# Kernel tuning notes

Hardware: AMD Instinct MI355X
Metric: run time of the kernel (lower is better)

The kernel has to match this reference:

```python
import jax, jax.numpy as jnp
import numpy as np

SCALE = 0.08838834764831845  # 1/sqrt(head_dim=128)
B, H, HKV, D = 32, 32, 8, 128
NUM_BLOCKS, BLOCK_SIZE, MAX_NUM_BLOCKS = 4096, 16, 256


def setup_inputs() -> dict:
    key = jax.random.key(0)
    ks = jax.random.split(key, 8)
    q = jax.random.normal(ks[0], (B, H, D), dtype=jnp.float32)
    k = jax.random.normal(ks[1], (B, HKV, D), dtype=jnp.float32)
    v = jax.random.normal(ks[2], (B, HKV, D), dtype=jnp.float32)
    k_cache = jax.random.normal(ks[3], (NUM_BLOCKS, BLOCK_SIZE, HKV, D), dtype=jnp.float32)
    v_cache = jax.random.normal(ks[4], (NUM_BLOCKS, BLOCK_SIZE, HKV, D), dtype=jnp.float32)
    slot_mapping = jax.random.randint(ks[5], (B,), 0, NUM_BLOCKS * BLOCK_SIZE, dtype=jnp.int32)
    block_tables = jax.random.randint(ks[6], (B, MAX_NUM_BLOCKS), 0, NUM_BLOCKS, dtype=jnp.int32)
    context_lens = jax.random.randint(ks[7], (B,), 0, MAX_NUM_BLOCKS * BLOCK_SIZE, dtype=jnp.int32)
    return {"q": q, "k": k, "v": v, "k_cache": k_cache, "v_cache": v_cache,
            "slot_mapping": slot_mapping, "block_tables": block_tables,
            "context_lens": context_lens}


def reference(q, k, v, k_cache, v_cache, slot_mapping, block_tables, context_lens):
    nb, bs, hkv, d = k_cache.shape
    b, h, _ = q.shape
    groups = h // hkv  # GQA repeat factor (repeat_interleave semantics)

    # --- store_kvcache: scatter the new decode token's k/v into the paged cache ---
    k_cache = k_cache.reshape(-1, hkv, d).at[slot_mapping].set(k).reshape(nb, bs, hkv, d)
    v_cache = v_cache.reshape(-1, hkv, d).at[slot_mapping].set(v).reshape(nb, bs, hkv, d)

    # --- block-table gather: [B, max_blocks] -> [B, T, HKV, D], T = max_blocks*bs ---
    t = block_tables.shape[1] * bs
    ids = jnp.maximum(block_tables, 0)  # clamp_min(0)
    k_tok = k_cache[ids].reshape(b, t, hkv, d)
    v_tok = v_cache[ids].reshape(b, t, hkv, d)

    # --- validity mask: block must be >=0 and token position < context_len ---
    pos = jnp.arange(t, dtype=jnp.int32)
    block_mask = jnp.repeat(block_tables >= 0, bs, axis=1)  # [B, T]
    valid = block_mask & (pos[None, :] < context_lens[:, None])
    has_tokens = valid.any(axis=1)  # [B]
    safe_valid = valid | ((~has_tokens)[:, None] & (pos[None, :] == 0))

    # --- attention (GQA via reshape instead of repeat_interleave materialization) ---
    qg = q.reshape(b, hkv, groups, d)  # head h = kv*groups + g matches repeat_interleave
    scores = jnp.einsum('bkgd,btkd->bkgt', qg, k_tok) * SCALE  # [B, HKV, G, T]
    scores = jnp.where(safe_valid[:, None, None, :], scores, -jnp.inf)
    w = jax.nn.softmax(scores.astype(jnp.float32), axis=-1).astype(q.dtype)
    o = jnp.einsum('bkgt,btkd->bkgd', w, v_tok).reshape(b, h, d)
    o = o * has_tokens[:, None, None].astype(o.dtype)
    return o[:, None, :, :]  # [B, 1, H, D] (matches transpose(1,2) of [B,H,1,D])
```

## Files before the change

kernel.cpp:

```cpp
#include <hip/hip_runtime.h>
#include <math.h>

#define B_ 32
#define H_ 32
#define HKV_ 8
#define G_ 4
#define D_ 128
#define BS_ 16
#define MAXNB_ 256
#define NPAGES_ 4096
#define NSLOTS_ (NPAGES_ * BS_)
#define PGSZ_ (BS_ * HKV_ * D_)
#define OVW_ 10
#define SC_ (0.08838834764831845f * 1.4426950408889634f)
#define NEG_ -1e30f

__global__ void build_slot_map(const int* __restrict__ slot_mapping,
                               const int* __restrict__ block_tables,
                               unsigned char* __restrict__ map,
                               unsigned int* __restrict__ pagemask,
                               unsigned int* __restrict__ ovr) {
  const int tid = threadIdx.x;
  uint4* m4 = (uint4*)map;
#pragma unroll
  for (int i = 0; i < NSLOTS_ / 16 / 256; ++i)
    m4[tid + i * 256] = make_uint4(0u, 0u, 0u, 0u);
  uint4* p4 = (uint4*)pagemask;
#pragma unroll
  for (int i = 0; i < NPAGES_ * 4 / 16 / 256; ++i)
    p4[tid + i * 256] = make_uint4(0u, 0u, 0u, 0u);
  for (int i = tid; i < B_ * OVW_; i += 256) ovr[i] = 0u;
  __syncthreads();
  if (tid == 0) {
#pragma unroll
    for (int j = 0; j < B_; ++j) {
      int s = slot_mapping[j];
      map[s] = (unsigned char)(j + 1);
      pagemask[s >> 4] |= (1u << (s & 15));
    }
  }
  __syncthreads();
  for (int e = tid; e < B_ * MAXNB_; e += 256) {
    int pgid = block_tables[e];
    if (pgid >= 0 && pgid < NPAGES_ && pagemask[pgid] != 0u) {
      int bb = e >> 8;
      int pos = e & 255;
      atomicOr(&ovr[bb * OVW_ + (pos >> 5)], 1u << (pos & 31));
    }
  }
}

__global__ __launch_bounds__(256, 4) void attn_split(
    const float* __restrict__ q,
    const float* __restrict__ k_new,
    const float* __restrict__ v_new,
    const float* __restrict__ k_cache,
    const float* __restrict__ v_cache,
    const int* __restrict__ block_tables,
    const int* __restrict__ context_lens,
    const unsigned char* __restrict__ map,
    const unsigned int* __restrict__ ovr,
    float* __restrict__ O_part,
    float* __restrict__ M_part,
    float* __restrict__ L_part,
    int nsplit)
{
  __shared__ float Ml[4][4];
  __shared__ float Ll[4][4];
  __shared__ float Ob[4][4][128];

  const int tid = threadIdx.x;
  const int tok = tid >> 4;
  const int c = tid & 15;

  const int s  = blockIdx.x % nsplit;
  const int bk = blockIdx.x / nsplit;
  const int kv = bk % HKV_;
  const int b  = bk / HKV_;

  float qr[G_][8];
#pragma unroll
  for (int g = 0; g < G_; ++g) {
    const float* qp = q + ((size_t)(b * H_ + kv * G_ + g)) * D_ + c * 8;
    float4 a0 = *(const float4*)qp;
    float4 a1 = *(const float4*)(qp + 4);
    qr[g][0] = a0.x * SC_; qr[g][1] = a0.y * SC_;
    qr[g][2] = a0.z * SC_; qr[g][3] = a0.w * SC_;
    qr[g][4] = a1.x * SC_; qr[g][5] = a1.y * SC_;
    qr[g][6] = a1.z * SC_; qr[g][7] = a1.w * SC_;
  }

  float m2[G_], l[G_], o[G_][8];
#pragma unroll
  for (int g = 0; g < G_; ++g) {
    m2[g] = NEG_; l[g] = 0.f;
#pragma unroll
    for (int j = 0; j < 8; ++j) o[g][j] = 0.f;
  }

  const int ctx = context_lens[b];
  const int pages_total = (ctx + BS_ - 1) / BS_;
  const int p_per = (pages_total + nsplit - 1) / nsplit;
  const int p0 = s * p_per;
  const int p1 = min(p0 + p_per, pages_total);

  const int toff = tok * (HKV_ * D_) + kv * D_ + c * 8;
  const int bt_base = b * MAXNB_;

  unsigned long long dwr;
  if (p_per <= 32) {
    const unsigned int* ow = ovr + b * OVW_;
    const int i0 = p0 >> 5, s0 = p0 & 31;
    unsigned long long lo = ow[i0], hi = ow[i0 + 1];
    dwr = ((hi << 32) | lo) >> s0;
  } else {
    dwr = ~0ull;
  }

  struct PBuf { float4 k0, k1, v0, v1; int blk; };
  PBuf A, B;

  auto fill = [&](PBuf& P, int id, bool ok) {
    P.blk = id;
    const int nb = id < 0 ? 0 : id;
    const float* kp = k_cache + (size_t)nb * PGSZ_ + toff;
    const float* vp = v_cache + (size_t)nb * PGSZ_ + toff;
    if (ok) {
      P.k0 = *(const float4*)kp; P.k1 = *(const float4*)(kp + 4);
      P.v0 = *(const float4*)vp; P.v1 = *(const float4*)(vp + 4);
    } else {
      P.k0 = P.k1 = P.v0 = P.v1 = make_float4(0.f, 0.f, 0.f, 0.f);
    }
  };

  auto step = [&](PBuf& P, int pgx, int nid, bool filln, bool chk) {
    const int thisblk = P.blk;
    if (chk) {
      const int bc0 = thisblk < 0 ? 0 : thisblk;
      const int mj = map[bc0 * BS_ + tok];
      if (mj != 0) {
        const int j = mj - 1;
        const float* kp = k_new + ((size_t)(j * HKV_ + kv)) * D_ + c * 8;
        const float* vp = v_new + ((size_t)(j * HKV_ + kv)) * D_ + c * 8;
        P.k0 = *(const float4*)kp; P.k1 = *(const float4*)(kp + 4);
        P.v0 = *(const float4*)vp; P.v1 = *(const float4*)(vp + 4);
      }
    }
    float dt[G_];
#pragma unroll
    for (int g = 0; g < G_; ++g) {
      dt[g] = qr[g][0] * P.k0.x + qr[g][1] * P.k0.y + qr[g][2] * P.k0.z + qr[g][3] * P.k0.w
            + qr[g][4] * P.k1.x + qr[g][5] * P.k1.y + qr[g][6] * P.k1.z + qr[g][7] * P.k1.w;
    }
    const int nb = nid < 0 ? 0 : nid;
    const float* nkp = k_cache + (size_t)nb * PGSZ_ + toff;
    const float* nvp = v_cache + (size_t)nb * PGSZ_ + toff;
    if (filln) { P.k0 = *(const float4*)nkp; P.k1 = *(const float4*)(nkp + 4); }
#pragma unroll
    for (int off = 1; off < 16; off <<= 1) {
#pragma unroll
      for (int g = 0; g < G_; ++g) dt[g] += __shfl_xor(dt[g], off, 16);
    }
    const int pos = pgx * BS_ + tok;
    if ((pos < ctx) && (thisblk >= 0)) {
#pragma unroll
      for (int g = 0; g < G_; ++g) {
        float t2 = dt[g];
        float mn = fmaxf(m2[g], t2);
        float al = exp2f(m2[g] - mn);
        float p  = exp2f(t2 - mn);
        l[g] = l[g] * al + p;
        m2[g] = mn;
        o[g][0] = o[g][0] * al + p * P.v0.x;
        o[g][1] = o[g][1] * al + p * P.v0.y;
        o[g][2] = o[g][2] * al + p * P.v0.z;
        o[g][3] = o[g][3] * al + p * P.v0.w;
        o[g][4] = o[g][4] * al + p * P.v1.x;
        o[g][5] = o[g][5] * al + p * P.v1.y;
        o[g][6] = o[g][6] * al + p * P.v1.z;
        o[g][7] = o[g][7] * al + p * P.v1.w;
      }
    }
    if (filln) { P.v0 = *(const float4*)nvp; P.v1 = *(const float4*)(nvp + 4); }
    P.blk = nid;
  };

  {
    int i0 = (p0 < p1) ? block_tables[bt_base + p0] : 0;
    int i1 = (p0 + 1 < p1) ? block_tables[bt_base + p0 + 1] : 0;
    fill(A, i0, p0 < p1);
    fill(B, i1, p0 + 1 < p1);
  }
  int nidA = (p0 + 2 < p1) ? block_tables[bt_base + p0 + 2] : 0;
  int nidB = (p0 + 3 < p1) ? block_tables[bt_base + p0 + 3] : 0;

  int pg = p0;
  for (; pg + 1 < p1; pg += 2) {
    step(A, pg,     nidA, pg + 2 < p1, (dwr & 1ull) != 0);
    step(B, pg + 1, nidB, pg + 3 < p1, (dwr & 2ull) != 0);
    nidA = (pg + 4 < p1) ? block_tables[bt_base + pg + 4] : 0;
    nidB = (pg + 5 < p1) ? block_tables[bt_base + pg + 5] : 0;
    dwr >>= 2;
  }
  if (pg < p1) step(A, pg, 0, false, (dwr & 1ull) != 0);

#pragma unroll
  for (int off = 16; off < 64; off <<= 1) {
#pragma unroll
    for (int g = 0; g < G_; ++g) {
      float mo = __shfl_xor(m2[g], off, 64);
      float lo = __shfl_xor(l[g], off, 64);
      float mn = fmaxf(m2[g], mo);
      float f1 = exp2f(m2[g] - mn);
      float f2 = exp2f(mo - mn);
      l[g] = f1 * l[g] + f2 * lo;
      m2[g] = mn;
#pragma unroll
      for (int j = 0; j < 8; ++j)
        o[g][j] = f1 * o[g][j] + f2 * __shfl_xor(o[g][j], off, 64);
    }
  }

  const int w = tid >> 6;
  if ((tid & 63) == 0) {
#pragma unroll
    for (int g = 0; g < G_; ++g) { Ml[w][g] = m2[g]; Ll[w][g] = l[g]; }
  }
  if (((tid >> 4) & 3) == 0) {
#pragma unroll
    for (int g = 0; g < G_; ++g) {
      float* dst = &Ob[w][g][c * 8];
      *(float4*)dst       = make_float4(o[g][0], o[g][1], o[g][2], o[g][3]);
      *(float4*)(dst + 4) = make_float4(o[g][4], o[g][5], o[g][6], o[g][7]);
    }
  }
  __syncthreads();

  const int g2 = tid >> 6;
  const int dd = (tid & 63) * 2;
  float M = NEG_;
#pragma unroll
  for (int wv = 0; wv < 4; ++wv) M = fmaxf(M, Ml[wv][g2]);
  float Ls = 0.f, a0 = 0.f, a1 = 0.f;
#pragma unroll
  for (int wv = 0; wv < 4; ++wv) {
    float f = exp2f(Ml[wv][g2] - M);
    Ls += f * Ll[wv][g2];
    float2 ov = *(const float2*)&Ob[wv][g2][dd];
    a0 += f * ov.x;
    a1 += f * ov.y;
  }
  const size_t pi = ((size_t)((b * HKV_ + kv) * G_ + g2) * nsplit + s);
  O_part[pi * D_ + dd]     = a0;
  O_part[pi * D_ + dd + 1] = a1;
  if (dd == 0) { M_part[pi] = M; L_part[pi] = Ls; }
}

__global__ void combine_splits(const float* __restrict__ O_part,
                               const float* __restrict__ M_part,
                               const float* __restrict__ L_part,
                               const int* __restrict__ context_lens,
                               float* __restrict__ out, int nsplit) {
  const int blk = blockIdx.x;
  const int b = blk >> 5;
  const int d = threadIdx.x;
  const int ctx = context_lens[b];
  float r = 0.f;
  if (ctx > 0) {
    const size_t base = (size_t)blk * nsplit;
    float M = NEG_;
    for (int s = 0; s < nsplit; ++s) M = fmaxf(M, M_part[base + s]);
    float den = 0.f, acc = 0.f;
    for (int s = 0; s < nsplit; ++s) {
      float f = exp2f(M_part[base + s] - M);
      den += f * L_part[base + s];
      acc += f * O_part[(base + s) * D_ + d];
    }
    r = den > 0.f ? acc / den : 0.f;
  }
  out[(size_t)blk * D_ + d] = r;
}

extern "C" void kernel_launch(void* const* d_in, const int* in_sizes, int n_in,
                              void* d_out, int out_size, void* d_ws, size_t ws_size,
                              hipStream_t stream) {
  const float* q = (const float*)d_in[0];
  const float* k = (const float*)d_in[1];
  const float* v = (const float*)d_in[2];
  const float* k_cache = (const float*)d_in[3];
  const float* v_cache = (const float*)d_in[4];
  const int* slot_mapping = (const int*)d_in[5];
  const int* block_tables = (const int*)d_in[6];
  const int* context_lens = (const int*)d_in[7];
  float* out = (float*)d_out;

  const size_t map_bytes = NSLOTS_;
  const size_t pmask_bytes = NPAGES_ * sizeof(unsigned int);
  const size_t ovr_bytes = 2048;
  unsigned char* map = (unsigned char*)d_ws;
  unsigned int* pagemask = (unsigned int*)((char*)d_ws + map_bytes);
  unsigned int* ovr = (unsigned int*)((char*)d_ws + map_bytes + pmask_bytes);

  int nsplit = 16;
  while (nsplit > 1) {
    size_t need = map_bytes + pmask_bytes + ovr_bytes +
                  (size_t)B_ * HKV_ * G_ * nsplit * (D_ + 2) * sizeof(float);
    if (need <= ws_size) break;
    nsplit >>= 1;
  }
  float* O_part = (float*)((char*)d_ws + map_bytes + pmask_bytes + ovr_bytes);
  float* M_part = O_part + (size_t)B_ * HKV_ * G_ * nsplit * D_;
  float* L_part = M_part + (size_t)B_ * HKV_ * G_ * nsplit;

  build_slot_map<<<1, 256, 0, stream>>>(slot_mapping, block_tables,
                                        map, pagemask, ovr);
  attn_split<<<B_ * HKV_ * nsplit, 256, 0, stream>>>(
      q, k, v, k_cache, v_cache, block_tables, context_lens, map, ovr,
      O_part, M_part, L_part, nsplit);
  combine_splits<<<B_ * H_, D_, 0, stream>>>(O_part, M_part, L_part,
                                             context_lens, out, nsplit);
}
```

Measured before the change: 537.2 us.

## Use one wavefront per split block processing whole pages with register prefetch

Rewrites the split attention kernel so that each workgroup is a single 64-lane wavefront. The wavefront handles all 16 tokens of a page in four groups of four, holding K/V for the current page in registers while the next page's loads are issued. This removes the LDS cross-wave reduction and the __syncthreads, and writes partials straight to global memory. nsplit is hardcoded to 16, which drops the workspace-size fallback and the dwr guard for p_per > 32. It raises register pressure and leaves fewer waves per workgroup, which could reduce the number of memory requests in flight.

```diff
diff --git a/kernel.cpp b/kernel.cpp
--- a/kernel.cpp
+++ b/kernel.cpp
@@ -11,6 +11,7 @@
 #define NPAGES_ 4096
 #define NSLOTS_ (NPAGES_ * BS_)
 #define PGSZ_ (BS_ * HKV_ * D_)
+#define NSPLIT_ 16
 #define OVW_ 10
 #define SC_ (0.08838834764831845f * 1.4426950408889634f)
 #define NEG_ -1e30f
@@ -50,7 +51,7 @@
   }
 }
 
-__global__ __launch_bounds__(256, 4) void attn_split(
+__global__ __launch_bounds__(64, 2) void attn_split(
     const float* __restrict__ q,
     const float* __restrict__ k_new,
     const float* __restrict__ v_new,
@@ -62,19 +63,14 @@
     const unsigned int* __restrict__ ovr,
     float* __restrict__ O_part,
     float* __restrict__ M_part,
-    float* __restrict__ L_part,
-    int nsplit)
+    float* __restrict__ L_part)
 {
-  __shared__ float Ml[4][4];
-  __shared__ float Ll[4][4];
-  __shared__ float Ob[4][4][128];
-
-  const int tid = threadIdx.x;
-  const int tok = tid >> 4;
-  const int c = tid & 15;
-
-  const int s  = blockIdx.x % nsplit;
-  const int bk = blockIdx.x / nsplit;
+  const int lane = threadIdx.x;
+  const int tg = lane >> 4;
+  const int c  = lane & 15;
+
+  const int s  = blockIdx.x % NSPLIT_;
+  const int bk = blockIdx.x / NSPLIT_;
   const int kv = bk % HKV_;
   const int b  = bk / HKV_;
 
@@ -100,109 +96,109 @@
 
   const int ctx = context_lens[b];
   const int pages_total = (ctx + BS_ - 1) / BS_;
-  const int p_per = (pages_total + nsplit - 1) / nsplit;
+  const int p_per = (pages_total + NSPLIT_ - 1) / NSPLIT_;
   const int p0 = s * p_per;
   const int p1 = min(p0 + p_per, pages_total);
-
-  const int toff = tok * (HKV_ * D_) + kv * D_ + c * 8;
   const int bt_base = b * MAXNB_;
 
+  const int loff = tg * (HKV_ * D_) + kv * D_ + c * 8;
+
   unsigned long long dwr;
-  if (p_per <= 32) {
+  {
     const unsigned int* ow = ovr + b * OVW_;
     const int i0 = p0 >> 5, s0 = p0 & 31;
     unsigned long long lo = ow[i0], hi = ow[i0 + 1];
     dwr = ((hi << 32) | lo) >> s0;
-  } else {
-    dwr = ~0ull;
-  }
-
-  struct PBuf { float4 k0, k1, v0, v1; int blk; };
-  PBuf A, B;
-
-  auto fill = [&](PBuf& P, int id, bool ok) {
-    P.blk = id;
-    const int nb = id < 0 ? 0 : id;
-    const float* kp = k_cache + (size_t)nb * PGSZ_ + toff;
-    const float* vp = v_cache + (size_t)nb * PGSZ_ + toff;
-    if (ok) {
-      P.k0 = *(const float4*)kp; P.k1 = *(const float4*)(kp + 4);
-      P.v0 = *(const float4*)vp; P.v1 = *(const float4*)(vp + 4);
-    } else {
-      P.k0 = P.k1 = P.v0 = P.v1 = make_float4(0.f, 0.f, 0.f, 0.f);
-    }
-  };
-
-  auto step = [&](PBuf& P, int pgx, int nid, bool filln, bool chk) {
-    const int thisblk = P.blk;
-    if (chk) {
-      const int bc0 = thisblk < 0 ? 0 : thisblk;
-      const int mj = map[bc0 * BS_ + tok];
-      if (mj != 0) {
-        const int j = mj - 1;
-        const float* kp = k_new + ((size_t)(j * HKV_ + kv)) * D_ + c * 8;
-        const float* vp = v_new + ((size_t)(j * HKV_ + kv)) * D_ + c * 8;
-        P.k0 = *(const float4*)kp; P.k1 = *(const float4*)(kp + 4);
-        P.v0 = *(const float4*)vp; P.v1 = *(const float4*)(vp + 4);
-      }
-    }
-    float dt[G_];
-#pragma unroll
-    for (int g = 0; g < G_; ++g) {
-      dt[g] = qr[g][0] * P.k0.x + qr[g][1] * P.k0.y + qr[g][2] * P.k0.z + qr[g][3] * P.k0.w
-            + qr[g][4] * P.k1.x + qr[g][5] * P.k1.y + qr[g][6] * P.k1.z + qr[g][7] * P.k1.w;
-    }
-    const int nb = nid < 0 ? 0 : nid;
-    const float* nkp = k_cache + (size_t)nb * PGSZ_ + toff;
-    const float* nvp = v_cache + (size_t)nb * PGSZ_ + toff;
-    if (filln) { P.k0 = *(const float4*)nkp; P.k1 = *(const float4*)(nkp + 4); }
-#pragma unroll
-    for (int off = 1; off < 16; off <<= 1) {
-#pragma unroll
-      for (int g = 0; g < G_; ++g) dt[g] += __shfl_xor(dt[g], off, 16);
-    }
-    const int pos = pgx * BS_ + tok;
-    if ((pos < ctx) && (thisblk >= 0)) {
+  }
+
+  float4 kk0[4], kk1[4], vv0[4], vv1[4];
+  int blkP = 0, blkN = 0;
+
+  if (p0 < p1) {
+    blkP = block_tables[bt_base + p0];
+    const int nb = blkP < 0 ? 0 : blkP;
+    const float* kb = k_cache + (size_t)nb * PGSZ_ + loff;
+    const float* vb = v_cache + (size_t)nb * PGSZ_ + loff;
+#pragma unroll
+    for (int X = 0; X < 4; ++X) {
+      const float* kp = kb + X * (4 * HKV_ * D_);
+      const float* vp = vb + X * (4 * HKV_ * D_);
+      kk0[X] = *(const float4*)kp; kk1[X] = *(const float4*)(kp + 4);
+      vv0[X] = *(const float4*)vp; vv1[X] = *(const float4*)(vp + 4);
+    }
+    blkN = (p0 + 1 < p1) ? block_tables[bt_base + p0 + 1] : 0;
+  }
+
+  for (int pg = p0; pg < p1; ++pg) {
+    if (dwr & 1ull) {
+      const int bc0 = blkP < 0 ? 0 : blkP;
+#pragma unroll
+      for (int X = 0; X < 4; ++X) {
+        const int mj = map[bc0 * BS_ + X * 4 + tg];
+        if (mj != 0) {
+          const int j = mj - 1;
+          const float* kp = k_new + ((size_t)(j * HKV_ + kv)) * D_ + c * 8;
+          const float* vp = v_new + ((size_t)(j * HKV_ + kv)) * D_ + c * 8;
+          kk0[X] = *(const float4*)kp; kk1[X] = *(const float4*)(kp + 4);
+          vv0[X] = *(const float4*)vp; vv1[X] = *(const float4*)(vp + 4);
+        }
+      }
+    }
+
+    const bool more = (pg + 1 < p1);
+    const int nb = blkN < 0 ? 0 : blkN;
+    const float* nkb = k_cache + (size_t)nb * PGSZ_ + loff;
+    const float* nvb = v_cache + (size_t)nb * PGSZ_ + loff;
+
+#pragma unroll
+    for (int X = 0; X < 4; ++X) {
+      float dt[G_];
 #pragma unroll
       for (int g = 0; g < G_; ++g) {
-        float t2 = dt[g];
-        float mn = fmaxf(m2[g], t2);
-        float al = exp2f(m2[g] - mn);
-        float p  = exp2f(t2 - mn);
-        l[g] = l[g] * al + p;
-        m2[g] = mn;
-        o[g][0] = o[g][0] * al + p * P.v0.x;
-        o[g][1] = o[g][1] * al + p * P.v0.y;
-        o[g][2] = o[g][2] * al + p * P.v0.z;
-        o[g][3] = o[g][3] * al + p * P.v0.w;
-        o[g][4] = o[g][4] * al + p * P.v1.x;
-        o[g][5] = o[g][5] * al + p * P.v1.y;
-        o[g][6] = o[g][6] * al + p * P.v1.z;
-        o[g][7] = o[g][7] * al + p * P.v1.w;
-      }
-    }
-    if (filln) { P.v0 = *(const float4*)nvp; P.v1 = *(const float4*)(nvp + 4); }
-    P.blk = nid;
-  };
-
-  {
-    int i0 = (p0 < p1) ? block_tables[bt_base + p0] : 0;
-    int i1 = (p0 + 1 < p1) ? block_tables[bt_base + p0 + 1] : 0;
-    fill(A, i0, p0 < p1);
-    fill(B, i1, p0 + 1 < p1);
-  }
-  int nidA = (p0 + 2 < p1) ? block_tables[bt_base + p0 + 2] : 0;
-  int nidB = (p0 + 3 < p1) ? block_tables[bt_base + p0 + 3] : 0;
-
-  int pg = p0;
-  for (; pg + 1 < p1; pg += 2) {
-    step(A, pg,     nidA, pg + 2 < p1, (dwr & 1ull) != 0);
-    step(B, pg + 1, nidB, pg + 3 < p1, (dwr & 2ull) != 0);
-    nidA = (pg + 4 < p1) ? block_tables[bt_base + pg + 4] : 0;
-    nidB = (pg + 5 < p1) ? block_tables[bt_base + pg + 5] : 0;
-    dwr >>= 2;
-  }
-  if (pg < p1) step(A, pg, 0, false, (dwr & 1ull) != 0);
+        dt[g] = qr[g][0] * kk0[X].x + qr[g][1] * kk0[X].y
+              + qr[g][2] * kk0[X].z + qr[g][3] * kk0[X].w
+              + qr[g][4] * kk1[X].x + qr[g][5] * kk1[X].y
+              + qr[g][6] * kk1[X].z + qr[g][7] * kk1[X].w;
+      }
+      if (more) {
+        const float* kp = nkb + X * (4 * HKV_ * D_);
+        kk0[X] = *(const float4*)kp; kk1[X] = *(const float4*)(kp + 4);
+      }
+#pragma unroll
+      for (int off = 1; off < 16; off <<= 1) {
+#pragma unroll
+        for (int g = 0; g < G_; ++g) dt[g] += __shfl_xor(dt[g], off, 16);
+      }
+      const int pos = pg * BS_ + X * 4 + tg;
+      if ((pos < ctx) && (blkP >= 0)) {
+#pragma unroll
+        for (int g = 0; g < G_; ++g) {
+          float t2 = dt[g];
+          float mn = fmaxf(m2[g], t2);
+          float al = exp2f(m2[g] - mn);
+          float p  = exp2f(t2 - mn);
+          l[g] = l[g] * al + p;
+          m2[g] = mn;
+          o[g][0] = o[g][0] * al + p * vv0[X].x;
+          o[g][1] = o[g][1] * al + p * vv0[X].y;
+          o[g][2] = o[g][2] * al + p * vv0[X].z;
+          o[g][3] = o[g][3] * al + p * vv0[X].w;
+          o[g][4] = o[g][4] * al + p * vv1[X].x;
+          o[g][5] = o[g][5] * al + p * vv1[X].y;
+          o[g][6] = o[g][6] * al + p * vv1[X].z;
+          o[g][7] = o[g][7] * al + p * vv1[X].w;
+        }
+      }
+      if (more) {
+        const float* vp = nvb + X * (4 * HKV_ * D_);
+        vv0[X] = *(const float4*)vp; vv1[X] = *(const float4*)(vp + 4);
+      }
+    }
+
+    blkP = blkN;
+    blkN = (pg + 2 < p1) ? block_tables[bt_base + pg + 2] : 0;
+    dwr >>= 1;
+  }
 
 #pragma unroll
   for (int off = 16; off < 64; off <<= 1) {
@@ -221,57 +217,36 @@
     }
   }
 
-  const int w = tid >> 6;
-  if ((tid & 63) == 0) {
-#pragma unroll
-    for (int g = 0; g < G_; ++g) { Ml[w][g] = m2[g]; Ll[w][g] = l[g]; }
-  }
-  if (((tid >> 4) & 3) == 0) {
+  if (lane < 16) {
 #pragma unroll
     for (int g = 0; g < G_; ++g) {
-      float* dst = &Ob[w][g][c * 8];
+      const size_t pi = ((size_t)((b * HKV_ + kv) * G_ + g) * NSPLIT_ + s);
+      float* dst = O_part + pi * D_ + c * 8;
       *(float4*)dst       = make_float4(o[g][0], o[g][1], o[g][2], o[g][3]);
       *(float4*)(dst + 4) = make_float4(o[g][4], o[g][5], o[g][6], o[g][7]);
-    }
-  }
-  __syncthreads();
-
-  const int g2 = tid >> 6;
-  const int dd = (tid & 63) * 2;
-  float M = NEG_;
-#pragma unroll
-  for (int wv = 0; wv < 4; ++wv) M = fmaxf(M, Ml[wv][g2]);
-  float Ls = 0.f, a0 = 0.f, a1 = 0.f;
-#pragma unroll
-  for (int wv = 0; wv < 4; ++wv) {
-    float f = exp2f(Ml[wv][g2] - M);
-    Ls += f * Ll[wv][g2];
-    float2 ov = *(const float2*)&Ob[wv][g2][dd];
-    a0 += f * ov.x;
-    a1 += f * ov.y;
-  }
-  const size_t pi = ((size_t)((b * HKV_ + kv) * G_ + g2) * nsplit + s);
-  O_part[pi * D_ + dd]     = a0;
-  O_part[pi * D_ + dd + 1] = a1;
-  if (dd == 0) { M_part[pi] = M; L_part[pi] = Ls; }
+      if (lane == 0) { M_part[pi] = m2[g]; L_part[pi] = l[g]; }
+    }
+  }
 }
 
 __global__ void combine_splits(const float* __restrict__ O_part,
                                const float* __restrict__ M_part,
                                const float* __restrict__ L_part,
                                const int* __restrict__ context_lens,
-                               float* __restrict__ out, int nsplit) {
+                               float* __restrict__ out) {
   const int blk = blockIdx.x;
   const int b = blk >> 5;
   const int d = threadIdx.x;
   const int ctx = context_lens[b];
   float r = 0.f;
   if (ctx > 0) {
-    const size_t base = (size_t)blk * nsplit;
+    const size_t base = (size_t)blk * NSPLIT_;
     float M = NEG_;
-    for (int s = 0; s < nsplit; ++s) M = fmaxf(M, M_part[base + s]);
+#pragma unroll
+    for (int s = 0; s < NSPLIT_; ++s) M = fmaxf(M, M_part[base + s]);
     float den = 0.f, acc = 0.f;
-    for (int s = 0; s < nsplit; ++s) {
+#pragma unroll
+    for (int s = 0; s < NSPLIT_; ++s) {
       float f = exp2f(M_part[base + s] - M);
       den += f * L_part[base + s];
       acc += f * O_part[(base + s) * D_ + d];
@@ -301,22 +276,15 @@
   unsigned int* pagemask = (unsigned int*)((char*)d_ws + map_bytes);
   unsigned int* ovr = (unsigned int*)((char*)d_ws + map_bytes + pmask_bytes);
 
-  int nsplit = 16;
-  while (nsplit > 1) {
-    size_t need = map_bytes + pmask_bytes + ovr_bytes +
-                  (size_t)B_ * HKV_ * G_ * nsplit * (D_ + 2) * sizeof(float);
-    if (need <= ws_size) break;
-    nsplit >>= 1;
-  }
   float* O_part = (float*)((char*)d_ws + map_bytes + pmask_bytes + ovr_bytes);
-  float* M_part = O_part + (size_t)B_ * HKV_ * G_ * nsplit * D_;
-  float* L_part = M_part + (size_t)B_ * HKV_ * G_ * nsplit;
+  float* M_part = O_part + (size_t)B_ * HKV_ * G_ * NSPLIT_ * D_;
+  float* L_part = M_part + (size_t)B_ * HKV_ * G_ * NSPLIT_;
 
   build_slot_map<<<1, 256, 0, stream>>>(slot_mapping, block_tables,
                                         map, pagemask, ovr);
-  attn_split<<<B_ * HKV_ * nsplit, 256, 0, stream>>>(
+  attn_split<<<B_ * HKV_ * NSPLIT_, 64, 0, stream>>>(
       q, k, v, k_cache, v_cache, block_tables, context_lens, map, ovr,
-      O_part, M_part, L_part, nsplit);
+      O_part, M_part, L_part);
   combine_splits<<<B_ * H_, D_, 0, stream>>>(O_part, M_part, L_part,
-                                             context_lens, out, nsplit);
-}
+                                             context_lens, out);
+}
```

New measurement: 551.0 us. +2.6%, slower.
